# Optimization experiments

Measured on AMD Instinct MI355X. Metric: run time of the kernel, lower is better.

## Reference

```python
import jax, jax.numpy as jnp
import numpy as np

N_NODES = 50000
N_EDGES = 600000
IN_DIM = 128
HID_DIM = 128


def setup_inputs() -> dict:
    key = jax.random.key(0)
    k_h, k_src, k_dst, k_w1, k_b1, k_w2, k_b2 = jax.random.split(key, 7)
    h = jax.random.normal(k_h, (N_NODES, IN_DIM), dtype=jnp.float32)
    src = jax.random.randint(k_src, (N_EDGES,), 0, N_NODES, dtype=jnp.int32)
    dst = jax.random.randint(k_dst, (N_EDGES,), 0, N_NODES, dtype=jnp.int32)
    # Edge MLP params: Linear(in_dim, out_dim) -> ReLU -> Linear(out_dim, 1) -> ReLU
    s1 = 1.0 / np.sqrt(IN_DIM)
    s2 = 1.0 / np.sqrt(HID_DIM)
    W1 = jax.random.uniform(k_w1, (IN_DIM, HID_DIM), jnp.float32, -s1, s1)
    b1 = jax.random.uniform(k_b1, (HID_DIM,), jnp.float32, -s1, s1)
    W2 = jax.random.uniform(k_w2, (HID_DIM, 1), jnp.float32, -s2, s2)
    b2 = jax.random.uniform(k_b2, (1,), jnp.float32, -s2, s2)
    return {"h": h, "src": src, "dst": dst, "W1": W1, "b1": b1, "W2": W2, "b2": b2}


def reference(h, src, dst, W1, b1, W2, b2):
    n_nodes = h.shape[0]
    # Edge MLP on feature differences (gather src/dst node features)
    dif = h[src] - h[dst]                                   # [E, D]
    hidden = jax.nn.relu(dif @ W1 + b1)                      # [E, H]
    att = jax.nn.relu(hidden @ W2 + b2)[:, 0]                # [E]
    att = jax.nn.sigmoid(att)                                # [E]
    # EdgeWeightNorm('right') on reversed graph: divide by the sum of
    # attention weights over edges sharing the same ORIGINAL source node.
    denom = jax.ops.segment_sum(att, src, num_segments=n_nodes)  # [N]
    w = att / denom[src]                                     # [E]
    # Message: w_e * src features, sum-aggregated at destination nodes
    msg = w[:, None] * h[src]                                # [E, D]
    out = jax.ops.segment_sum(msg, dst, num_segments=n_nodes)  # [N, D]
    return out
```

## Files before the change

kernel.cpp:

```cpp
#include <hip/hip_runtime.h>
#include <hip/hip_fp8.h>


typedef unsigned int uint;
typedef unsigned short ushort;
typedef unsigned char uchar;
typedef __attribute__((ext_vector_type(8))) short short8;
typedef __attribute__((ext_vector_type(4))) float f32x4;
typedef __attribute__((ext_vector_type(2))) float f32x2;

static __device__ __forceinline__ uint pack_f16(float a, float b) {
  _Float16 ha = (_Float16)a, hb = (_Float16)b;
  unsigned short ua = __builtin_bit_cast(unsigned short, ha);
  unsigned short ub = __builtin_bit_cast(unsigned short, hb);
  return ((uint)ub << 16) | ua;
}
static __device__ __forceinline__ float2 unpack_f16(uint u) {
  _Float16 lo = __builtin_bit_cast(_Float16, (unsigned short)(u & 0xffffu));
  _Float16 hi = __builtin_bit_cast(_Float16, (unsigned short)(u >> 16));
  return make_float2((float)lo, (float)hi);
}
static __device__ __forceinline__ ushort f2bf(float x) {
  uint u = __float_as_uint(x);
  u += 0x7fffu + ((u >> 16) & 1u);
  return (ushort)(u >> 16);
}

#if __has_builtin(__builtin_amdgcn_cvt_pk_fp8_f32) && __has_builtin(__builtin_amdgcn_cvt_pk_f32_fp8)
static __device__ __forceinline__ uchar f2fp8(float v) {
  uint u = __builtin_amdgcn_cvt_pk_fp8_f32(v, v, 0u, false);
  return (uchar)(u & 0xFFu);
}
template <bool HI>
static __device__ __forceinline__ float2 fp8x2(uint word) {
  f32x2 r = __builtin_amdgcn_cvt_pk_f32_fp8(word, HI);
  return make_float2(r.x, r.y);
}
#else
static __device__ __forceinline__ uchar f2fp8(float v) {
  __hip_fp8_e4m3 t(v);
  return *(uchar*)&t;
}
static __device__ __forceinline__ float fp8one(uchar b) {
  __hip_fp8_e4m3 t;
  *(uchar*)&t = b;
  return (float)t;
}
template <bool HI>
static __device__ __forceinline__ float2 fp8x2(uint word) {
  uint sh = HI ? 16 : 0;
  return make_float2(fp8one((uchar)(word >> sh)), fp8one((uchar)(word >> (sh + 8))));
}
#endif

static __device__ __forceinline__ float dpp_red16(float x) {
  int v;
  v = __builtin_amdgcn_update_dpp(0, __builtin_bit_cast(int, x), 0xB1, 0xF, 0xF, true);
  x += __builtin_bit_cast(float, v);
  v = __builtin_amdgcn_update_dpp(0, __builtin_bit_cast(int, x), 0x4E, 0xF, 0xF, true);
  x += __builtin_bit_cast(float, v);
  v = __builtin_amdgcn_update_dpp(0, __builtin_bit_cast(int, x), 0x124, 0xF, 0xF, true);
  x += __builtin_bit_cast(float, v);
  v = __builtin_amdgcn_update_dpp(0, __builtin_bit_cast(int, x), 0x128, 0xF, 0xF, true);
  x += __builtin_bit_cast(float, v);
  return x;
}

__global__ __launch_bounds__(256) void k_prep(const float* __restrict__ W1,
                                              ushort* __restrict__ w1t_swz,
                                              int* __restrict__ zbase, int zwords) {
  int b = blockIdx.x;
  if (b < 64) {
    int idx = b * 256 + threadIdx.x;
    int n = idx >> 7, k = idx & 127;
    float v = W1[k * 128 + n];
    int byte_off = n * 256 + ((k * 2) ^ ((n & 7) << 4));
    w1t_swz[byte_off >> 1] = f2bf(v);
  } else {
    int i = (b - 64) * 256 + threadIdx.x;
    int stride = (gridDim.x - 64) * 256;
    for (; i < zwords; i += stride) zbase[i] = 0;
  }
}

__global__ __launch_bounds__(256) void k_gemm(const float* __restrict__ h,
                                              const ushort* __restrict__ w1t_swz,
                                              uchar* __restrict__ gh8,
                                              uint4* __restrict__ hh4,
                                              int n_nodes,
                                              const int* __restrict__ dst,
                                              int* __restrict__ counts,
                                              int* __restrict__ rank,
                                              int n_edges, int gemm_blocks) {
  if ((int)blockIdx.x >= gemm_blocks) {
    int hb = blockIdx.x - gemm_blocks;
    int i = hb * 256 + threadIdx.x;
    int stride = (gridDim.x - gemm_blocks) * 256;
    for (int e = i; e < n_edges; e += stride) {
      int r = atomicAdd(&counts[dst[e]], 1);
      rank[e] = r;
    }
    return;
  }
  __shared__ ushort w1s[16384];
  int tid = threadIdx.x;
  {
    const uint4* srcw = (const uint4*)w1t_swz;
    uint4* dstw = (uint4*)w1s;
    #pragma unroll
    for (int i = 0; i < 8; ++i) dstw[tid + 256 * i] = srcw[tid + 256 * i];
  }
  __syncthreads();
  int wave = tid >> 6, lane = tid & 63;
  int tile = blockIdx.x * 4 + wave;
  if (tile * 16 >= n_nodes) return;
  int n0 = tile * 16;
  int l15 = lane & 15, kq = lane >> 4;
  int row = n0 + l15;

  f32x4 acc[8];
  #pragma unroll
  for (int ct = 0; ct < 8; ++ct) acc[ct] = (f32x4){0.f, 0.f, 0.f, 0.f};

  #pragma unroll
  for (int kb = 0; kb < 4; ++kb) {
    const float* hp = &h[(size_t)row * 128 + kb * 32 + kq * 8];
    float4 p0 = *(const float4*)hp;
    float4 p1 = *(const float4*)(hp + 4);
    short8 a;
    a[0] = (short)f2bf(p0.x); a[1] = (short)f2bf(p0.y);
    a[2] = (short)f2bf(p0.z); a[3] = (short)f2bf(p0.w);
    a[4] = (short)f2bf(p1.x); a[5] = (short)f2bf(p1.y);
    a[6] = (short)f2bf(p1.z); a[7] = (short)f2bf(p1.w);
    uint4 hv;
    hv.x = pack_f16(p0.x, p0.y); hv.y = pack_f16(p0.z, p0.w);
    hv.z = pack_f16(p1.x, p1.y); hv.w = pack_f16(p1.z, p1.w);
    hh4[(size_t)row * 16 + kb * 4 + kq] = hv;
    #pragma unroll
    for (int ct = 0; ct < 8; ++ct) {
      int n = ct * 16 + l15;
      int byte_off = n * 256 + (((kb * 64) + kq * 16) ^ ((n & 7) << 4));
      short8 b = *(const short8*)((const char*)w1s + byte_off);
      acc[ct] = __builtin_amdgcn_mfma_f32_16x16x32_bf16(a, b, acc[ct], 0, 0, 0);
    }
  }
  #pragma unroll
  for (int ct = 0; ct < 8; ++ct) {
    #pragma unroll
    for (int r = 0; r < 4; ++r) {
      int orow = n0 + kq * 4 + r;
      gh8[(size_t)orow * 128 + ct * 16 + l15] = f2fp8(acc[ct][r]);
    }
  }
}

__global__ __launch_bounds__(256) void k_scanA(const int* __restrict__ counts,
                                               int* __restrict__ partials,
                                               int n, int chunk) {
  __shared__ int red[256];
  int b = blockIdx.x, t = threadIdx.x;
  int idx = b * chunk + t;
  red[t] = (t < chunk && idx < n) ? counts[idx] : 0;
  __syncthreads();
  for (int off = 128; off > 0; off >>= 1) {
    if (t < off) red[t] += red[t + off];
    __syncthreads();
  }
  if (t == 0) partials[b] = red[0];
}

__global__ __launch_bounds__(256) void k_scanC2(const int* __restrict__ counts,
                                                const int* __restrict__ partials,
                                                int* __restrict__ row_start,
                                                int n, int chunk, int total) {
  __shared__ int bp[256];
  __shared__ int p[256];
  int b = blockIdx.x, t = threadIdx.x;
  bp[t] = partials[t];
  __syncthreads();
  #pragma unroll
  for (int off = 1; off < 256; off <<= 1) {
    int v = (t >= off) ? bp[t - off] : 0;
    __syncthreads();
    bp[t] += v;
    __syncthreads();
  }
  int base = (b == 0) ? 0 : bp[b - 1];
  int idx = b * chunk + t;
  bool ok = (t < chunk && idx < n);
  int orig = ok ? counts[idx] : 0;
  p[t] = orig;
  __syncthreads();
  #pragma unroll
  for (int off = 1; off < 256; off <<= 1) {
    int v = (t >= off) ? p[t - off] : 0;
    __syncthreads();
    p[t] += v;
    __syncthreads();
  }
  if (ok) row_start[idx] = base + p[t] - orig;
  if (b == 0 && t == 0) row_start[n] = total;
}

__global__ __launch_bounds__(256) void k_fill0(const int* __restrict__ src,
                                               const int* __restrict__ dst,
                                               const int* __restrict__ row_start,
                                               const int* __restrict__ rank,
                                               int* __restrict__ bsrc,
                                               int n_edges) {
  int i = blockIdx.x * blockDim.x + threadIdx.x;
  int stride = gridDim.x * blockDim.x;
  for (int e = i; e < n_edges; e += stride) {
    bsrc[row_start[dst[e]] + rank[e]] = src[e];
  }
}

__global__ __launch_bounds__(256) void k_att2(const uint2* __restrict__ gh8v,
                                              const int* __restrict__ bsrc,
                                              const int* __restrict__ row_start,
                                              const float* __restrict__ b1,
                                              const float* __restrict__ W2,
                                              const float* __restrict__ b2,
                                              int2* __restrict__ bucket,
                                              float* __restrict__ denom,
                                              int n_nodes) {
  int lane = threadIdx.x & 63;
  int sub = lane >> 4, l16 = lane & 15;
  int wavei = threadIdx.x >> 6;
  int d = blockIdx.x * 16 + wavei * 4 + sub;
  int beg = 0, end = 0;
  if (d < n_nodes) { beg = row_start[d]; end = row_start[d + 1]; }
  float4 b1a = *(const float4*)&b1[l16 * 8];
  float4 b1b = *(const float4*)&b1[l16 * 8 + 4];
  float4 w2a = *(const float4*)&W2[l16 * 8];
  float4 w2b = *(const float4*)&W2[l16 * 8 + 4];
  float b2v = b2[0];
  float c0 = 0.f, c1 = 0.f, c2 = 0.f, c3 = 0.f;
  float c4 = 0.f, c5 = 0.f, c6 = 0.f, c7 = 0.f;
  if (beg < end) {
    uint2 ud = gh8v[(size_t)d * 16 + l16];
    float2 da = fp8x2<false>(ud.x), db = fp8x2<true>(ud.x);
    float2 dc = fp8x2<false>(ud.y), dd = fp8x2<true>(ud.y);
    c0 = b1a.x - da.x; c1 = b1a.y - da.y; c2 = b1a.z - db.x; c3 = b1a.w - db.y;
    c4 = b1b.x - dc.x; c5 = b1b.y - dc.y; c6 = b1b.z - dd.x; c7 = b1b.w - dd.y;
  }
  for (int j0 = beg; j0 < end; j0 += 2) {
    int j1 = j0 + 1;
    bool v1 = j1 < end;
    int s0 = bsrc[j0];
    int s1 = v1 ? bsrc[j1] : 0;
    uint2 ua = gh8v[(size_t)s0 * 16 + l16];
    uint2 ub;
    if (v1) ub = gh8v[(size_t)s1 * 16 + l16];
    float acc0 = 0.f, acc1 = 0.f;
    {
      float2 f0 = fp8x2<false>(ua.x), f1 = fp8x2<true>(ua.x);
      float2 f2 = fp8x2<false>(ua.y), f3 = fp8x2<true>(ua.y);
      float t;
      t = fmaxf(f0.x + c0, 0.f); acc0 = fmaf(t, w2a.x, acc0);
      t = fmaxf(f0.y + c1, 0.f); acc0 = fmaf(t, w2a.y, acc0);
      t = fmaxf(f1.x + c2, 0.f); acc0 = fmaf(t, w2a.z, acc0);
      t = fmaxf(f1.y + c3, 0.f); acc0 = fmaf(t, w2a.w, acc0);
      t = fmaxf(f2.x + c4, 0.f); acc0 = fmaf(t, w2b.x, acc0);
      t = fmaxf(f2.y + c5, 0.f); acc0 = fmaf(t, w2b.y, acc0);
      t = fmaxf(f3.x + c6, 0.f); acc0 = fmaf(t, w2b.z, acc0);
      t = fmaxf(f3.y + c7, 0.f); acc0 = fmaf(t, w2b.w, acc0);
    }
    if (v1) {
      float2 f0 = fp8x2<false>(ub.x), f1 = fp8x2<true>(ub.x);
      float2 f2 = fp8x2<false>(ub.y), f3 = fp8x2<true>(ub.y);
      float t;
      t = fmaxf(f0.x + c0, 0.f); acc1 = fmaf(t, w2a.x, acc1);
      t = fmaxf(f0.y + c1, 0.f); acc1 = fmaf(t, w2a.y, acc1);
      t = fmaxf(f1.x + c2, 0.f); acc1 = fmaf(t, w2a.z, acc1);
      t = fmaxf(f1.y + c3, 0.f); acc1 = fmaf(t, w2a.w, acc1);
      t = fmaxf(f2.x + c4, 0.f); acc1 = fmaf(t, w2b.x, acc1);
      t = fmaxf(f2.y + c5, 0.f); acc1 = fmaf(t, w2b.y, acc1);
      t = fmaxf(f3.x + c6, 0.f); acc1 = fmaf(t, w2b.z, acc1);
      t = fmaxf(f3.y + c7, 0.f); acc1 = fmaf(t, w2b.w, acc1);
    }
    acc0 = dpp_red16(acc0);
    acc1 = dpp_red16(acc1);
    if (l16 == 0) {
      float a = fmaxf(acc0 + b2v, 0.f);
      a = 1.f / (1.f + __expf(-a));
      bucket[j0] = make_int2(s0, __float_as_int(a));
      atomicAdd(&denom[s0], a);
      if (v1) {
        float a1 = fmaxf(acc1 + b2v, 0.f);
        a1 = 1.f / (1.f + __expf(-a1));
        bucket[j1] = make_int2(s1, __float_as_int(a1));
        atomicAdd(&denom[s1], a1);
      }
    }
  }
}

__global__ __launch_bounds__(256) void k_agg(const uint4* __restrict__ hh4,
                                             const int* __restrict__ row_start,
                                             const int2* __restrict__ bucket,
                                             const float* __restrict__ denom,
                                             float* __restrict__ out, int n_nodes) {
  int lane = threadIdx.x & 63;
  int sub = lane >> 4, l16 = lane & 15;
  int wavei = threadIdx.x >> 6;
  int d = blockIdx.x * 16 + wavei * 4 + sub;
  int beg = 0, end = 0;
  if (d < n_nodes) { beg = row_start[d]; end = row_start[d + 1]; }
  float a0 = 0.f, a1 = 0.f, a2 = 0.f, a3 = 0.f;
  float a4 = 0.f, a5 = 0.f, a6 = 0.f, a7 = 0.f;
  for (int j0 = beg; j0 < end; j0 += 2) {
    int j1 = j0 + 1;
    bool v1 = j1 < end;
    int2 e0 = bucket[j0];
    int2 e1 = v1 ? bucket[j1] : make_int2(0, 0);
    float w0 = __int_as_float(e0.y) / denom[e0.x];
    float w1 = v1 ? __int_as_float(e1.y) / denom[e1.x] : 0.f;
    uint4 va = hh4[(size_t)e0.x * 16 + l16];
    uint4 vb;
    if (v1) vb = hh4[(size_t)e1.x * 16 + l16];
    {
      float2 f0 = unpack_f16(va.x), f1 = unpack_f16(va.y);
      float2 f2 = unpack_f16(va.z), f3 = unpack_f16(va.w);
      a0 = fmaf(w0, f0.x, a0); a1 = fmaf(w0, f0.y, a1);
      a2 = fmaf(w0, f1.x, a2); a3 = fmaf(w0, f1.y, a3);
      a4 = fmaf(w0, f2.x, a4); a5 = fmaf(w0, f2.y, a5);
      a6 = fmaf(w0, f3.x, a6); a7 = fmaf(w0, f3.y, a7);
    }
    if (v1) {
      float2 f0 = unpack_f16(vb.x), f1 = unpack_f16(vb.y);
      float2 f2 = unpack_f16(vb.z), f3 = unpack_f16(vb.w);
      a0 = fmaf(w1, f0.x, a0); a1 = fmaf(w1, f0.y, a1);
      a2 = fmaf(w1, f1.x, a2); a3 = fmaf(w1, f1.y, a3);
      a4 = fmaf(w1, f2.x, a4); a5 = fmaf(w1, f2.y, a5);
      a6 = fmaf(w1, f3.x, a6); a7 = fmaf(w1, f3.y, a7);
    }
  }
  if (d < n_nodes) {
    *(float4*)&out[(size_t)d * 128 + l16 * 8]     = make_float4(a0, a1, a2, a3);
    *(float4*)&out[(size_t)d * 128 + l16 * 8 + 4] = make_float4(a4, a5, a6, a7);
  }
}

extern "C" void kernel_launch(void* const* d_in, const int* in_sizes, int n_in,
                              void* d_out, int out_size, void* d_ws, size_t ws_size,
                              hipStream_t stream) {
  const float* h   = (const float*)d_in[0];
  const int*   src = (const int*)d_in[1];
  const int*   dst = (const int*)d_in[2];
  const float* W1  = (const float*)d_in[3];
  const float* b1  = (const float*)d_in[4];
  const float* W2  = (const float*)d_in[5];
  const float* b2  = (const float*)d_in[6];
  float* out = (float*)d_out;

  int n_nodes = in_sizes[0] / 128;
  int n_edges = in_sizes[1];

  char* ws = (char*)d_ws;
  uchar*  gh8       = (uchar*)ws;
  uint*   hh        = (uint*)(ws + (size_t)n_nodes * 128);
  float*  denom     = (float*)(hh + (size_t)n_nodes * 64);
  int*    counts    = (int*)(denom + n_nodes);
  int*    row_start = counts + n_nodes;
  int*    partials  = row_start + n_nodes + 1;
  ushort* w1t       = (ushort*)(partials + 256);
  int*    bsrc      = (int*)(w1t + 16384);
  int*    rank      = bsrc + n_edges;
  int2*   bucket    = (int2*)(((uintptr_t)(rank + n_edges) + 15) & ~(uintptr_t)15);

  int chunk = (n_nodes + 255) / 256;
  int n_tiles = (n_nodes + 15) / 16;
  int gemm_blocks = (n_tiles + 3) / 4;
  int nblk16 = (n_nodes + 15) / 16;
  k_prep  <<<64 + 16, 256, 0, stream>>>(W1, w1t, (int*)denom, 2 * n_nodes);
  k_gemm  <<<gemm_blocks + 256, 256, 0, stream>>>(h, w1t, gh8, (uint4*)hh, n_nodes,
                                                  dst, counts, rank, n_edges, gemm_blocks);
  k_scanA <<<256, 256, 0, stream>>>(counts, partials, n_nodes, chunk);
  k_scanC2<<<256, 256, 0, stream>>>(counts, partials, row_start, n_nodes, chunk, n_edges);
  k_fill0 <<<1024, 256, 0, stream>>>(src, dst, row_start, rank, bsrc, n_edges);
  k_att2  <<<nblk16, 256, 0, stream>>>((const uint2*)gh8, bsrc, row_start, b1, W2, b2,
                                       bucket, denom, n_nodes);
  k_agg   <<<nblk16, 256, 0, stream>>>((const uint4*)hh, row_start, bucket, denom, out, n_nodes);
}
```

Measured before the change: 134.0 us.

## Unroll edge loops by eight and prescale source features by inverse denominator

The attention and aggregation loops now process eight edges per iteration, issuing all gathers before compute to raise memory-level parallelism. Over-reads past the segment end are clamped to a valid node index and masked out. A new k_norm kernel divides the fp16 source feature rows by their denominator once per node, which removes the per-edge division and denom gather from k_agg. The workspace is reordered so reads past the end of bucket land inside bsrc. This costs an extra pass over the fp16 features and an fp16 rounding of the scaled values.

```diff
diff --git a/kernel.cpp b/kernel.cpp
--- a/kernel.cpp
+++ b/kernel.cpp
@@ -64,6 +64,34 @@
   v = __builtin_amdgcn_update_dpp(0, __builtin_bit_cast(int, x), 0x128, 0xF, 0xF, true);
   x += __builtin_bit_cast(float, v);
   return x;
+}
+
+struct AttC { float c0, c1, c2, c3, c4, c5, c6, c7; float4 w2a, w2b; };
+
+static __device__ __forceinline__ float edge_logit(uint2 u, const AttC& k) {
+  float2 f0 = fp8x2<false>(u.x), f1 = fp8x2<true>(u.x);
+  float2 f2 = fp8x2<false>(u.y), f3 = fp8x2<true>(u.y);
+  float acc = 0.f, t;
+  t = fmaxf(f0.x + k.c0, 0.f); acc = fmaf(t, k.w2a.x, acc);
+  t = fmaxf(f0.y + k.c1, 0.f); acc = fmaf(t, k.w2a.y, acc);
+  t = fmaxf(f1.x + k.c2, 0.f); acc = fmaf(t, k.w2a.z, acc);
+  t = fmaxf(f1.y + k.c3, 0.f); acc = fmaf(t, k.w2a.w, acc);
+  t = fmaxf(f2.x + k.c4, 0.f); acc = fmaf(t, k.w2b.x, acc);
+  t = fmaxf(f2.y + k.c5, 0.f); acc = fmaf(t, k.w2b.y, acc);
+  t = fmaxf(f3.x + k.c6, 0.f); acc = fmaf(t, k.w2b.z, acc);
+  t = fmaxf(f3.y + k.c7, 0.f); acc = fmaf(t, k.w2b.w, acc);
+  return acc;
+}
+
+static __device__ __forceinline__ void accv(float wgt, uint4 row,
+                                            float& a0, float& a1, float& a2, float& a3,
+                                            float& a4, float& a5, float& a6, float& a7) {
+  float2 f0 = unpack_f16(row.x), f1 = unpack_f16(row.y);
+  float2 f2 = unpack_f16(row.z), f3 = unpack_f16(row.w);
+  a0 = fmaf(wgt, f0.x, a0); a1 = fmaf(wgt, f0.y, a1);
+  a2 = fmaf(wgt, f1.x, a2); a3 = fmaf(wgt, f1.y, a3);
+  a4 = fmaf(wgt, f2.x, a4); a5 = fmaf(wgt, f2.y, a5);
+  a6 = fmaf(wgt, f3.x, a6); a7 = fmaf(wgt, f3.y, a7);
 }
 
 __global__ __launch_bounds__(256) void k_prep(const float* __restrict__ W1,
@@ -232,74 +260,80 @@
   if (d < n_nodes) { beg = row_start[d]; end = row_start[d + 1]; }
   float4 b1a = *(const float4*)&b1[l16 * 8];
   float4 b1b = *(const float4*)&b1[l16 * 8 + 4];
-  float4 w2a = *(const float4*)&W2[l16 * 8];
-  float4 w2b = *(const float4*)&W2[l16 * 8 + 4];
+  AttC K;
+  K.w2a = *(const float4*)&W2[l16 * 8];
+  K.w2b = *(const float4*)&W2[l16 * 8 + 4];
   float b2v = b2[0];
-  float c0 = 0.f, c1 = 0.f, c2 = 0.f, c3 = 0.f;
-  float c4 = 0.f, c5 = 0.f, c6 = 0.f, c7 = 0.f;
+  K.c0 = K.c1 = K.c2 = K.c3 = K.c4 = K.c5 = K.c6 = K.c7 = 0.f;
   if (beg < end) {
     uint2 ud = gh8v[(size_t)d * 16 + l16];
     float2 da = fp8x2<false>(ud.x), db = fp8x2<true>(ud.x);
     float2 dc = fp8x2<false>(ud.y), dd = fp8x2<true>(ud.y);
-    c0 = b1a.x - da.x; c1 = b1a.y - da.y; c2 = b1a.z - db.x; c3 = b1a.w - db.y;
-    c4 = b1b.x - dc.x; c5 = b1b.y - dc.y; c6 = b1b.z - dd.x; c7 = b1b.w - dd.y;
-  }
-  for (int j0 = beg; j0 < end; j0 += 2) {
-    int j1 = j0 + 1;
-    bool v1 = j1 < end;
-    int s0 = bsrc[j0];
-    int s1 = v1 ? bsrc[j1] : 0;
-    uint2 ua = gh8v[(size_t)s0 * 16 + l16];
-    uint2 ub;
-    if (v1) ub = gh8v[(size_t)s1 * 16 + l16];
-    float acc0 = 0.f, acc1 = 0.f;
-    {
-      float2 f0 = fp8x2<false>(ua.x), f1 = fp8x2<true>(ua.x);
-      float2 f2 = fp8x2<false>(ua.y), f3 = fp8x2<true>(ua.y);
-      float t;
-      t = fmaxf(f0.x + c0, 0.f); acc0 = fmaf(t, w2a.x, acc0);
-      t = fmaxf(f0.y + c1, 0.f); acc0 = fmaf(t, w2a.y, acc0);
-      t = fmaxf(f1.x + c2, 0.f); acc0 = fmaf(t, w2a.z, acc0);
-      t = fmaxf(f1.y + c3, 0.f); acc0 = fmaf(t, w2a.w, acc0);
-      t = fmaxf(f2.x + c4, 0.f); acc0 = fmaf(t, w2b.x, acc0);
-      t = fmaxf(f2.y + c5, 0.f); acc0 = fmaf(t, w2b.y, acc0);
-      t = fmaxf(f3.x + c6, 0.f); acc0 = fmaf(t, w2b.z, acc0);
-      t = fmaxf(f3.y + c7, 0.f); acc0 = fmaf(t, w2b.w, acc0);
-    }
-    if (v1) {
-      float2 f0 = fp8x2<false>(ub.x), f1 = fp8x2<true>(ub.x);
-      float2 f2 = fp8x2<false>(ub.y), f3 = fp8x2<true>(ub.y);
-      float t;
-      t = fmaxf(f0.x + c0, 0.f); acc1 = fmaf(t, w2a.x, acc1);
-      t = fmaxf(f0.y + c1, 0.f); acc1 = fmaf(t, w2a.y, acc1);
-      t = fmaxf(f1.x + c2, 0.f); acc1 = fmaf(t, w2a.z, acc1);
-      t = fmaxf(f1.y + c3, 0.f); acc1 = fmaf(t, w2a.w, acc1);
-      t = fmaxf(f2.x + c4, 0.f); acc1 = fmaf(t, w2b.x, acc1);
-      t = fmaxf(f2.y + c5, 0.f); acc1 = fmaf(t, w2b.y, acc1);
-      t = fmaxf(f3.x + c6, 0.f); acc1 = fmaf(t, w2b.z, acc1);
-      t = fmaxf(f3.y + c7, 0.f); acc1 = fmaf(t, w2b.w, acc1);
-    }
-    acc0 = dpp_red16(acc0);
-    acc1 = dpp_red16(acc1);
+    K.c0 = b1a.x - da.x; K.c1 = b1a.y - da.y; K.c2 = b1a.z - db.x; K.c3 = b1a.w - db.y;
+    K.c4 = b1b.x - dc.x; K.c5 = b1b.y - dc.y; K.c6 = b1b.z - dd.x; K.c7 = b1b.w - dd.y;
+  }
+  uint nn = (uint)n_nodes;
+  for (int base = beg; base < end; base += 8) {
+    int s0 = bsrc[base + 0], s1 = bsrc[base + 1];
+    int s2 = bsrc[base + 2], s3 = bsrc[base + 3];
+    int s4 = bsrc[base + 4], s5 = bsrc[base + 5];
+    int s6 = bsrc[base + 6], s7 = bsrc[base + 7];
+    s0 = ((uint)s0 < nn) ? s0 : 0;  s1 = ((uint)s1 < nn) ? s1 : 0;
+    s2 = ((uint)s2 < nn) ? s2 : 0;  s3 = ((uint)s3 < nn) ? s3 : 0;
+    s4 = ((uint)s4 < nn) ? s4 : 0;  s5 = ((uint)s5 < nn) ? s5 : 0;
+    s6 = ((uint)s6 < nn) ? s6 : 0;  s7 = ((uint)s7 < nn) ? s7 : 0;
+    uint2 u0 = gh8v[(size_t)s0 * 16 + l16];
+    uint2 u1 = gh8v[(size_t)s1 * 16 + l16];
+    uint2 u2 = gh8v[(size_t)s2 * 16 + l16];
+    uint2 u3 = gh8v[(size_t)s3 * 16 + l16];
+    uint2 u4 = gh8v[(size_t)s4 * 16 + l16];
+    uint2 u5 = gh8v[(size_t)s5 * 16 + l16];
+    uint2 u6 = gh8v[(size_t)s6 * 16 + l16];
+    uint2 u7 = gh8v[(size_t)s7 * 16 + l16];
+    float a0 = dpp_red16(edge_logit(u0, K));
+    float a1 = dpp_red16(edge_logit(u1, K));
+    float a2 = dpp_red16(edge_logit(u2, K));
+    float a3 = dpp_red16(edge_logit(u3, K));
+    float a4 = dpp_red16(edge_logit(u4, K));
+    float a5 = dpp_red16(edge_logit(u5, K));
+    float a6 = dpp_red16(edge_logit(u6, K));
+    float a7 = dpp_red16(edge_logit(u7, K));
     if (l16 == 0) {
-      float a = fmaxf(acc0 + b2v, 0.f);
-      a = 1.f / (1.f + __expf(-a));
-      bucket[j0] = make_int2(s0, __float_as_int(a));
-      atomicAdd(&denom[s0], a);
-      if (v1) {
-        float a1 = fmaxf(acc1 + b2v, 0.f);
-        a1 = 1.f / (1.f + __expf(-a1));
-        bucket[j1] = make_int2(s1, __float_as_int(a1));
-        atomicAdd(&denom[s1], a1);
+      float aa[8] = {a0, a1, a2, a3, a4, a5, a6, a7};
+      int ss[8] = {s0, s1, s2, s3, s4, s5, s6, s7};
+      #pragma unroll
+      for (int j = 0; j < 8; ++j) {
+        if (base + j < end) {
+          float a = fmaxf(aa[j] + b2v, 0.f);
+          a = 1.f / (1.f + __expf(-a));
+          bucket[base + j] = make_int2(ss[j], __float_as_int(a));
+          atomicAdd(&denom[ss[j]], a);
+        }
       }
     }
   }
+}
+
+__global__ __launch_bounds__(256) void k_norm(uint4* __restrict__ hh4,
+                                              const float* __restrict__ denom,
+                                              int n_nodes) {
+  int i = blockIdx.x * 256 + threadIdx.x;
+  if (i >= n_nodes * 16) return;
+  int node = i >> 4;
+  float inv = 1.f / denom[node];
+  uint4 v = hh4[i];
+  float2 f0 = unpack_f16(v.x), f1 = unpack_f16(v.y);
+  float2 f2 = unpack_f16(v.z), f3 = unpack_f16(v.w);
+  v.x = pack_f16(f0.x * inv, f0.y * inv);
+  v.y = pack_f16(f1.x * inv, f1.y * inv);
+  v.z = pack_f16(f2.x * inv, f2.y * inv);
+  v.w = pack_f16(f3.x * inv, f3.y * inv);
+  hh4[i] = v;
 }
 
 __global__ __launch_bounds__(256) void k_agg(const uint4* __restrict__ hh4,
                                              const int* __restrict__ row_start,
                                              const int2* __restrict__ bucket,
-                                             const float* __restrict__ denom,
                                              float* __restrict__ out, int n_nodes) {
   int lane = threadIdx.x & 63;
   int sub = lane >> 4, l16 = lane & 15;
@@ -309,32 +343,40 @@
   if (d < n_nodes) { beg = row_start[d]; end = row_start[d + 1]; }
   float a0 = 0.f, a1 = 0.f, a2 = 0.f, a3 = 0.f;
   float a4 = 0.f, a5 = 0.f, a6 = 0.f, a7 = 0.f;
-  for (int j0 = beg; j0 < end; j0 += 2) {
-    int j1 = j0 + 1;
-    bool v1 = j1 < end;
-    int2 e0 = bucket[j0];
-    int2 e1 = v1 ? bucket[j1] : make_int2(0, 0);
-    float w0 = __int_as_float(e0.y) / denom[e0.x];
-    float w1 = v1 ? __int_as_float(e1.y) / denom[e1.x] : 0.f;
-    uint4 va = hh4[(size_t)e0.x * 16 + l16];
-    uint4 vb;
-    if (v1) vb = hh4[(size_t)e1.x * 16 + l16];
-    {
-      float2 f0 = unpack_f16(va.x), f1 = unpack_f16(va.y);
-      float2 f2 = unpack_f16(va.z), f3 = unpack_f16(va.w);
-      a0 = fmaf(w0, f0.x, a0); a1 = fmaf(w0, f0.y, a1);
-      a2 = fmaf(w0, f1.x, a2); a3 = fmaf(w0, f1.y, a3);
-      a4 = fmaf(w0, f2.x, a4); a5 = fmaf(w0, f2.y, a5);
-      a6 = fmaf(w0, f3.x, a6); a7 = fmaf(w0, f3.y, a7);
-    }
-    if (v1) {
-      float2 f0 = unpack_f16(vb.x), f1 = unpack_f16(vb.y);
-      float2 f2 = unpack_f16(vb.z), f3 = unpack_f16(vb.w);
-      a0 = fmaf(w1, f0.x, a0); a1 = fmaf(w1, f0.y, a1);
-      a2 = fmaf(w1, f1.x, a2); a3 = fmaf(w1, f1.y, a3);
-      a4 = fmaf(w1, f2.x, a4); a5 = fmaf(w1, f2.y, a5);
-      a6 = fmaf(w1, f3.x, a6); a7 = fmaf(w1, f3.y, a7);
-    }
+  uint nn = (uint)n_nodes;
+  for (int base = beg; base < end; base += 8) {
+    int2 e0 = bucket[base + 0], e1 = bucket[base + 1];
+    int2 e2 = bucket[base + 2], e3 = bucket[base + 3];
+    int2 e4 = bucket[base + 4], e5 = bucket[base + 5];
+    int2 e6 = bucket[base + 6], e7 = bucket[base + 7];
+    int s0 = ((uint)e0.x < nn) ? e0.x : 0;  int s1 = ((uint)e1.x < nn) ? e1.x : 0;
+    int s2 = ((uint)e2.x < nn) ? e2.x : 0;  int s3 = ((uint)e3.x < nn) ? e3.x : 0;
+    int s4 = ((uint)e4.x < nn) ? e4.x : 0;  int s5 = ((uint)e5.x < nn) ? e5.x : 0;
+    int s6 = ((uint)e6.x < nn) ? e6.x : 0;  int s7 = ((uint)e7.x < nn) ? e7.x : 0;
+    uint4 v0 = hh4[(size_t)s0 * 16 + l16];
+    uint4 v1 = hh4[(size_t)s1 * 16 + l16];
+    uint4 v2 = hh4[(size_t)s2 * 16 + l16];
+    uint4 v3 = hh4[(size_t)s3 * 16 + l16];
+    uint4 v4 = hh4[(size_t)s4 * 16 + l16];
+    uint4 v5 = hh4[(size_t)s5 * 16 + l16];
+    uint4 v6 = hh4[(size_t)s6 * 16 + l16];
+    uint4 v7 = hh4[(size_t)s7 * 16 + l16];
+    float w0 = (base + 0 < end) ? __int_as_float(e0.y) : 0.f;
+    float w1 = (base + 1 < end) ? __int_as_float(e1.y) : 0.f;
+    float w2 = (base + 2 < end) ? __int_as_float(e2.y) : 0.f;
+    float w3 = (base + 3 < end) ? __int_as_float(e3.y) : 0.f;
+    float w4 = (base + 4 < end) ? __int_as_float(e4.y) : 0.f;
+    float w5 = (base + 5 < end) ? __int_as_float(e5.y) : 0.f;
+    float w6 = (base + 6 < end) ? __int_as_float(e6.y) : 0.f;
+    float w7 = (base + 7 < end) ? __int_as_float(e7.y) : 0.f;
+    accv(w0, v0, a0, a1, a2, a3, a4, a5, a6, a7);
+    accv(w1, v1, a0, a1, a2, a3, a4, a5, a6, a7);
+    accv(w2, v2, a0, a1, a2, a3, a4, a5, a6, a7);
+    accv(w3, v3, a0, a1, a2, a3, a4, a5, a6, a7);
+    accv(w4, v4, a0, a1, a2, a3, a4, a5, a6, a7);
+    accv(w5, v5, a0, a1, a2, a3, a4, a5, a6, a7);
+    accv(w6, v6, a0, a1, a2, a3, a4, a5, a6, a7);
+    accv(w7, v7, a0, a1, a2, a3, a4, a5, a6, a7);
   }
   if (d < n_nodes) {
     *(float4*)&out[(size_t)d * 128 + l16 * 8]     = make_float4(a0, a1, a2, a3);
@@ -365,9 +407,9 @@
   int*    row_start = counts + n_nodes;
   int*    partials  = row_start + n_nodes + 1;
   ushort* w1t       = (ushort*)(partials + 256);
-  int*    bsrc      = (int*)(w1t + 16384);
+  int2*   bucket    = (int2*)(((uintptr_t)(w1t + 16384) + 15) & ~(uintptr_t)15);
+  int*    bsrc      = (int*)(bucket + n_edges);
   int*    rank      = bsrc + n_edges;
-  int2*   bucket    = (int2*)(((uintptr_t)(rank + n_edges) + 15) & ~(uintptr_t)15);
 
   int chunk = (n_nodes + 255) / 256;
   int n_tiles = (n_nodes + 15) / 16;
@@ -381,5 +423,6 @@
   k_fill0 <<<1024, 256, 0, stream>>>(src, dst, row_start, rank, bsrc, n_edges);
   k_att2  <<<nblk16, 256, 0, stream>>>((const uint2*)gh8, bsrc, row_start, b1, W2, b2,
                                        bucket, denom, n_nodes);
-  k_agg   <<<nblk16, 256, 0, stream>>>((const uint4*)hh, row_start, bucket, denom, out, n_nodes);
-}
+  k_norm  <<<(n_nodes * 16 + 255) / 256, 256, 0, stream>>>((uint4*)hh, denom, n_nodes);
+  k_agg   <<<nblk16, 256, 0, stream>>>((const uint4*)hh, row_start, bucket, out, n_nodes);
+}
```

Measured after the change: 131.7 us, median of 2. Within noise of the previous version (-1.7%).
